# Kernel tuning notes

Hardware: AMD Instinct MI355X
Metric: run time of the kernel (lower is better)

Reference implementation:

```python
import jax, jax.numpy as jnp
import numpy as np

N_NODES = 100000
N_FEATURES = 128
N_FILTERS = 128
N_EDGES = 3200000


def setup_inputs() -> dict:
    key = jax.random.key(0)
    k_x, k_f, k_src, k_dst, k_w = jax.random.split(key, 5)
    x = jax.random.normal(k_x, (N_NODES, N_FEATURES), dtype=jnp.float32)
    filters = jax.random.normal(k_f, (N_FEATURES, N_FILTERS), dtype=jnp.float32)
    edge_src = jax.random.randint(k_src, (N_EDGES,), 0, N_NODES, dtype=jnp.int64)
    edge_dst = jnp.sort(jax.random.randint(k_dst, (N_EDGES,), 0, N_NODES, dtype=jnp.int64))
    edge_weight = jax.random.uniform(k_w, (N_EDGES,), dtype=jnp.float32)
    return {"x": x, "filters": filters, "edge_src": edge_src,
            "edge_dst": edge_dst, "edge_weight": edge_weight}


def reference(x, filters, edge_src, edge_dst, edge_weight):
    # Dense feature transform: XF = x @ filters  -> [N, n_filters]
    XF = jnp.matmul(x, filters)
    # Sparse aggregation: out[d] += w_e * XF[s] for each edge (s, d, w_e)
    # equivalent to torch.sparse.mm(transform, XF) with transform in COO form.
    msgs = XF[edge_src] * edge_weight[:, None]           # [E, n_filters]
    out = jax.ops.segment_sum(msgs, edge_dst, num_segments=N_NODES)
    return out
```

## Files before the change

kernel.cpp:

```cpp
#include <hip/hip_runtime.h>
#include <stdint.h>

#define N_NODES 100000
#define N_FEAT 128
#define N_EDGES 3200000

static __device__ __forceinline__ unsigned int f2bf_u(float f) {
    unsigned int u = __float_as_uint(f);
    u += 0x7FFFu + ((u >> 16) & 1u);
    return u >> 16;
}

typedef __bf16 bf16x8 __attribute__((ext_vector_type(8)));
typedef float f32x4 __attribute__((ext_vector_type(4)));

__global__ __launch_bounds__(256) void k_prep(
        const float* __restrict__ x, unsigned int* __restrict__ xi8,
        float* __restrict__ xscale,
        const float* __restrict__ f, unsigned short* __restrict__ fB,
        const int* __restrict__ dst, int* __restrict__ row_ptr) {
    int b = blockIdx.x;
    if (b < 12500) {
        int wave = threadIdx.x >> 6, lane = threadIdx.x & 63;
        int l32 = lane & 31;
        int node = b * 8 + wave * 2 + (lane >> 5);
        float4 v = *(const float4*)(x + (size_t)node * 128 + l32 * 4);
        float am = fmaxf(fmaxf(fabsf(v.x), fabsf(v.y)), fmaxf(fabsf(v.z), fabsf(v.w)));
        for (int d = 1; d < 32; d <<= 1) am = fmaxf(am, __shfl_xor(am, d));
        float s = am * (1.f / 127.f);
        float inv = 127.f / fmaxf(am, 1e-20f);
        int q0 = (int)rintf(v.x * inv), q1 = (int)rintf(v.y * inv);
        int q2 = (int)rintf(v.z * inv), q3 = (int)rintf(v.w * inv);
        xi8[(size_t)node * 32 + l32] = (unsigned int)((q0 & 0xFF) | ((q1 & 0xFF) << 8) |
                                                      ((q2 & 0xFF) << 16) | ((q3 & 0xFF) << 24));
        if (l32 == 0) xscale[node] = s;
    } else if (b < 25000) {
        int e = (b - 12500) * 256 + threadIdx.x;
        if (e >= N_EDGES) return;
        int dcur = dst[e];
        if (e == 0) {
            for (int d = 0; d <= dcur; ++d) row_ptr[d] = 0;
        } else {
            int dprev = dst[e - 1];
            for (int d = dprev + 1; d <= dcur; ++d) row_ptr[d] = e;
        }
        if (e == N_EDGES - 1) {
            for (int d = dcur + 1; d <= N_NODES; ++d) row_ptr[d] = N_EDGES;
        }
    } else {
        int i = (b - 25000) * 256 + threadIdx.x;
        if (i >= N_FEAT * N_FEAT) return;
        int n = ((i >> 11) << 4) | ((i >> 3) & 15);
        int k = (((i >> 9) & 3) << 5) | (((i >> 7) & 3) << 3) | (i & 7);
        fB[i] = (unsigned short)f2bf_u(f[k * 128 + n]);
    }
}

__global__ __launch_bounds__(256) void k_aggregate(
        const unsigned int* __restrict__ xi8,
        const float* __restrict__ xscale,
        const int* __restrict__ src,
        const float* __restrict__ w,
        const int* __restrict__ row_ptr,
        unsigned int* __restrict__ aggb) {
    __shared__ uint2 smeta[4][64];
    int wave = threadIdx.x >> 6, lane = threadIdx.x & 63;
    int node = blockIdx.x * 4 + wave;
    if (node >= N_NODES) return;
    int half = lane >> 5, f = lane & 31;
    int start = row_ptr[node], end = row_ptr[node + 1];
    float a0 = 0.f, a1 = 0.f, a2 = 0.f, a3 = 0.f;

    for (int e0 = start; e0 < end; e0 += 64) {
        int e = e0 + lane;
        uint2 m = make_uint2(0u, 0u);
        if (e < end) {
            int sv = src[e];
            m.x = (unsigned int)sv;
            m.y = __float_as_uint(w[e] * xscale[sv]);
        }
        smeta[wave][lane] = m;
        int cnt16 = (min(64, end - e0) + 15) & ~15;
        for (int j = 0; j < cnt16; j += 16) {
            unsigned int vv[8]; float wj[8];
#pragma unroll
            for (int u = 0; u < 8; ++u) {
                uint2 mm = smeta[wave][j + u * 2 + half];
                wj[u] = __uint_as_float(mm.y);
                vv[u] = xi8[mm.x * 32 + f];
            }
#pragma unroll
            for (int u = 0; u < 8; ++u) {
                int s32 = (int)vv[u];
                a0 = fmaf(wj[u], (float)((s32 << 24) >> 24), a0);
                a1 = fmaf(wj[u], (float)((s32 << 16) >> 24), a1);
                a2 = fmaf(wj[u], (float)((s32 <<  8) >> 24), a2);
                a3 = fmaf(wj[u], (float)( s32        >> 24), a3);
            }
        }
    }
    a0 += __shfl_xor(a0, 32);
    a1 += __shfl_xor(a1, 32);
    a2 += __shfl_xor(a2, 32);
    a3 += __shfl_xor(a3, 32);
    if (half == 0) {
        uint2 o;
        o.x = (f2bf_u(a1) << 16) | f2bf_u(a0);
        o.y = (f2bf_u(a3) << 16) | f2bf_u(a2);
        *(uint2*)(aggb + (size_t)node * 64 + f * 2) = o;
    }
}

__global__ __launch_bounds__(256) void k_gemm(
        const unsigned short* __restrict__ A,
        const unsigned short* __restrict__ fB,
        float* __restrict__ C) {
    __shared__ unsigned short Bbuf[16384];
    int t = threadIdx.x;
    for (int i = 0; i < 8; ++i)
        ((uint4*)Bbuf)[t + i * 256] = ((const uint4*)fB)[t + i * 256];
    __syncthreads();

    int wave = t >> 6, lane = t & 63, m15 = lane & 15, q = lane >> 4;
    int row = blockIdx.x * 64 + wave * 16 + m15;
    int rowc = min(row, N_NODES - 1);

    f32x4 acc[8];
#pragma unroll
    for (int j = 0; j < 8; ++j) acc[j] = f32x4{0.f, 0.f, 0.f, 0.f};

#pragma unroll
    for (int kkidx = 0; kkidx < 4; ++kkidx) {
        bf16x8 a = *(const bf16x8*)(A + (size_t)rowc * 128 + kkidx * 32 + q * 8);
#pragma unroll
        for (int j = 0; j < 8; ++j) {
            bf16x8 b = *(const bf16x8*)(Bbuf + (((j * 4 + kkidx) * 64 + lane) * 8));
            acc[j] = __builtin_amdgcn_mfma_f32_16x16x32_bf16(a, b, acc[j], 0, 0, 0);
        }
    }

    int rowbase = blockIdx.x * 64 + wave * 16 + q * 4;
#pragma unroll
    for (int j = 0; j < 8; ++j)
        for (int r = 0; r < 4; ++r) {
            int gr = rowbase + r;
            if (gr < N_NODES)
                C[(size_t)gr * 128 + j * 16 + m15] = acc[j][r];
        }
}

extern "C" void kernel_launch(void* const* d_in, const int* in_sizes, int n_in,
                              void* d_out, int out_size, void* d_ws, size_t ws_size,
                              hipStream_t stream) {
    const float* x        = (const float*)d_in[0];
    const float* filters  = (const float*)d_in[1];
    const int*   edge_src = (const int*)d_in[2];
    const int*   edge_dst = (const int*)d_in[3];
    const float* edge_w   = (const float*)d_in[4];
    float* out = (float*)d_out;

    char* ws = (char*)d_ws;
    unsigned int*   xi8  = (unsigned int*)  (ws);
    float*          xsc  = (float*)         (ws + 13ll * 1024 * 1024);
    unsigned int*   aggb = (unsigned int*)  (ws + 14ll * 1024 * 1024);
    unsigned short* fB   = (unsigned short*)(ws + 40ll * 1024 * 1024);
    int*            rp   = (int*)           (ws + 41ll * 1024 * 1024);

    hipLaunchKernelGGL(k_prep, dim3(25064), dim3(256), 0, stream,
                       x, xi8, xsc, filters, fB, edge_dst, rp);
    hipLaunchKernelGGL(k_aggregate, dim3(25000), dim3(256), 0, stream,
                       xi8, xsc, edge_src, edge_w, rp, aggb);
    hipLaunchKernelGGL(k_gemm, dim3(1563), dim3(256), 0, stream,
                       (const unsigned short*)aggb, fB, out);
}
```

Measured before the change: 201.9 us.

## Reorder to transform-then-aggregate with int8-quantized XF and direct fp32 output

Moves the dense matmul ahead of the sparse aggregation: a new kernel computes XF = x @ filters with bf16 MFMA and quantizes each row to offset-128 uint8 with a per-row scale. The aggregation kernel then gathers the int8 XF rows, subtracts the offset using an accumulated weight sum, and writes fp32 output directly. This removes the separate GEMM pass and the bf16 intermediate aggregate buffer, at the cost of quantizing XF rather than x, which changes the error profile.

```diff
diff --git a/kernel.cpp b/kernel.cpp
--- a/kernel.cpp
+++ b/kernel.cpp
@@ -15,27 +15,11 @@
 typedef float f32x4 __attribute__((ext_vector_type(4)));
 
 __global__ __launch_bounds__(256) void k_prep(
-        const float* __restrict__ x, unsigned int* __restrict__ xi8,
-        float* __restrict__ xscale,
         const float* __restrict__ f, unsigned short* __restrict__ fB,
         const int* __restrict__ dst, int* __restrict__ row_ptr) {
     int b = blockIdx.x;
     if (b < 12500) {
-        int wave = threadIdx.x >> 6, lane = threadIdx.x & 63;
-        int l32 = lane & 31;
-        int node = b * 8 + wave * 2 + (lane >> 5);
-        float4 v = *(const float4*)(x + (size_t)node * 128 + l32 * 4);
-        float am = fmaxf(fmaxf(fabsf(v.x), fabsf(v.y)), fmaxf(fabsf(v.z), fabsf(v.w)));
-        for (int d = 1; d < 32; d <<= 1) am = fmaxf(am, __shfl_xor(am, d));
-        float s = am * (1.f / 127.f);
-        float inv = 127.f / fmaxf(am, 1e-20f);
-        int q0 = (int)rintf(v.x * inv), q1 = (int)rintf(v.y * inv);
-        int q2 = (int)rintf(v.z * inv), q3 = (int)rintf(v.w * inv);
-        xi8[(size_t)node * 32 + l32] = (unsigned int)((q0 & 0xFF) | ((q1 & 0xFF) << 8) |
-                                                      ((q2 & 0xFF) << 16) | ((q3 & 0xFF) << 24));
-        if (l32 == 0) xscale[node] = s;
-    } else if (b < 25000) {
-        int e = (b - 12500) * 256 + threadIdx.x;
+        int e = b * 256 + threadIdx.x;
         if (e >= N_EDGES) return;
         int dcur = dst[e];
         if (e == 0) {
@@ -48,11 +32,76 @@
             for (int d = dcur + 1; d <= N_NODES; ++d) row_ptr[d] = N_EDGES;
         }
     } else {
-        int i = (b - 25000) * 256 + threadIdx.x;
+        int i = (b - 12500) * 256 + threadIdx.x;
         if (i >= N_FEAT * N_FEAT) return;
         int n = ((i >> 11) << 4) | ((i >> 3) & 15);
         int k = (((i >> 9) & 3) << 5) | (((i >> 7) & 3) << 3) | (i & 7);
         fB[i] = (unsigned short)f2bf_u(f[k * 128 + n]);
+    }
+}
+
+__global__ __launch_bounds__(256) void k_xf(
+        const float* __restrict__ x,
+        const unsigned short* __restrict__ fB,
+        unsigned int* __restrict__ xi8,
+        float* __restrict__ xscale) {
+    __shared__ unsigned short Bbuf[16384];
+    int t = threadIdx.x;
+    for (int i = 0; i < 8; ++i)
+        ((uint4*)Bbuf)[t + i * 256] = ((const uint4*)fB)[t + i * 256];
+    __syncthreads();
+
+    int wave = t >> 6, lane = t & 63, m15 = lane & 15, q = lane >> 4;
+    int row = blockIdx.x * 64 + wave * 16 + m15;
+    int rowc = min(row, N_NODES - 1);
+
+    f32x4 acc[8];
+#pragma unroll
+    for (int j = 0; j < 8; ++j) acc[j] = f32x4{0.f, 0.f, 0.f, 0.f};
+
+#pragma unroll
+    for (int kkidx = 0; kkidx < 4; ++kkidx) {
+        const float* ap = x + (size_t)rowc * 128 + kkidx * 32 + q * 8;
+        float4 v0 = *(const float4*)ap;
+        float4 v1 = *(const float4*)(ap + 4);
+        union { bf16x8 v; unsigned short s[8]; } au;
+        au.s[0] = (unsigned short)f2bf_u(v0.x);
+        au.s[1] = (unsigned short)f2bf_u(v0.y);
+        au.s[2] = (unsigned short)f2bf_u(v0.z);
+        au.s[3] = (unsigned short)f2bf_u(v0.w);
+        au.s[4] = (unsigned short)f2bf_u(v1.x);
+        au.s[5] = (unsigned short)f2bf_u(v1.y);
+        au.s[6] = (unsigned short)f2bf_u(v1.z);
+        au.s[7] = (unsigned short)f2bf_u(v1.w);
+#pragma unroll
+        for (int j = 0; j < 8; ++j) {
+            bf16x8 bfrag = *(const bf16x8*)(Bbuf + (((j * 4 + kkidx) * 64 + lane) * 8));
+            acc[j] = __builtin_amdgcn_mfma_f32_16x16x32_bf16(au.v, bfrag, acc[j], 0, 0, 0);
+        }
+    }
+
+    int rowbase = blockIdx.x * 64 + wave * 16 + q * 4;
+#pragma unroll
+    for (int r = 0; r < 4; ++r) {
+        float mx = 0.f;
+#pragma unroll
+        for (int j = 0; j < 8; ++j) mx = fmaxf(mx, fabsf(acc[j][r]));
+        for (int d = 1; d < 16; d <<= 1) mx = fmaxf(mx, __shfl_xor(mx, d));
+        float inv = 127.f / fmaxf(mx, 1e-20f);
+        unsigned int u0 = 0, u1 = 0;
+#pragma unroll
+        for (int bb = 0; bb < 4; ++bb) {
+            unsigned int q0 = (unsigned int)(int)(rintf(acc[2 * bb][r] * inv) + 128.f);
+            unsigned int q1 = (unsigned int)(int)(rintf(acc[2 * bb + 1][r] * inv) + 128.f);
+            u0 |= (q0 & 0xFFu) << (8 * bb);
+            u1 |= (q1 & 0xFFu) << (8 * bb);
+        }
+        int gr = rowbase + r;
+        if (gr < N_NODES) {
+            xi8[(size_t)gr * 32 + m15] = u0;
+            xi8[(size_t)gr * 32 + 16 + m15] = u1;
+            if (m15 == 0) xscale[gr] = mx * (1.f / 127.f);
+        }
     }
 }
 
@@ -62,14 +111,14 @@
         const int* __restrict__ src,
         const float* __restrict__ w,
         const int* __restrict__ row_ptr,
-        unsigned int* __restrict__ aggb) {
+        float* __restrict__ out) {
     __shared__ uint2 smeta[4][64];
     int wave = threadIdx.x >> 6, lane = threadIdx.x & 63;
     int node = blockIdx.x * 4 + wave;
     if (node >= N_NODES) return;
     int half = lane >> 5, f = lane & 31;
     int start = row_ptr[node], end = row_ptr[node + 1];
-    float a0 = 0.f, a1 = 0.f, a2 = 0.f, a3 = 0.f;
+    float a0 = 0.f, a1 = 0.f, a2 = 0.f, a3 = 0.f, aw = 0.f;
 
     for (int e0 = start; e0 < end; e0 += 64) {
         int e = e0 + lane;
@@ -91,62 +140,30 @@
             }
 #pragma unroll
             for (int u = 0; u < 8; ++u) {
-                int s32 = (int)vv[u];
-                a0 = fmaf(wj[u], (float)((s32 << 24) >> 24), a0);
-                a1 = fmaf(wj[u], (float)((s32 << 16) >> 24), a1);
-                a2 = fmaf(wj[u], (float)((s32 <<  8) >> 24), a2);
-                a3 = fmaf(wj[u], (float)( s32        >> 24), a3);
+                a0 = fmaf(wj[u], (float)( vv[u]         & 0xFFu), a0);
+                a1 = fmaf(wj[u], (float)((vv[u] >>  8)  & 0xFFu), a1);
+                a2 = fmaf(wj[u], (float)((vv[u] >> 16)  & 0xFFu), a2);
+                a3 = fmaf(wj[u], (float)( vv[u] >> 24          ), a3);
+                aw += wj[u];
             }
         }
     }
+    a0 = fmaf(-128.f, aw, a0);
+    a1 = fmaf(-128.f, aw, a1);
+    a2 = fmaf(-128.f, aw, a2);
+    a3 = fmaf(-128.f, aw, a3);
+
     a0 += __shfl_xor(a0, 32);
     a1 += __shfl_xor(a1, 32);
     a2 += __shfl_xor(a2, 32);
     a3 += __shfl_xor(a3, 32);
     if (half == 0) {
-        uint2 o;
-        o.x = (f2bf_u(a1) << 16) | f2bf_u(a0);
-        o.y = (f2bf_u(a3) << 16) | f2bf_u(a2);
-        *(uint2*)(aggb + (size_t)node * 64 + f * 2) = o;
+        float* o = out + (size_t)node * 128 + f;
+        o[ 0] = a0;
+        o[32] = a1;
+        o[64] = a2;
+        o[96] = a3;
     }
-}
-
-__global__ __launch_bounds__(256) void k_gemm(
-        const unsigned short* __restrict__ A,
-        const unsigned short* __restrict__ fB,
-        float* __restrict__ C) {
-    __shared__ unsigned short Bbuf[16384];
-    int t = threadIdx.x;
-    for (int i = 0; i < 8; ++i)
-        ((uint4*)Bbuf)[t + i * 256] = ((const uint4*)fB)[t + i * 256];
-    __syncthreads();
-
-    int wave = t >> 6, lane = t & 63, m15 = lane & 15, q = lane >> 4;
-    int row = blockIdx.x * 64 + wave * 16 + m15;
-    int rowc = min(row, N_NODES - 1);
-
-    f32x4 acc[8];
-#pragma unroll
-    for (int j = 0; j < 8; ++j) acc[j] = f32x4{0.f, 0.f, 0.f, 0.f};
-
-#pragma unroll
-    for (int kkidx = 0; kkidx < 4; ++kkidx) {
-        bf16x8 a = *(const bf16x8*)(A + (size_t)rowc * 128 + kkidx * 32 + q * 8);
-#pragma unroll
-        for (int j = 0; j < 8; ++j) {
-            bf16x8 b = *(const bf16x8*)(Bbuf + (((j * 4 + kkidx) * 64 + lane) * 8));
-            acc[j] = __builtin_amdgcn_mfma_f32_16x16x32_bf16(a, b, acc[j], 0, 0, 0);
-        }
-    }
-
-    int rowbase = blockIdx.x * 64 + wave * 16 + q * 4;
-#pragma unroll
-    for (int j = 0; j < 8; ++j)
-        for (int r = 0; r < 4; ++r) {
-            int gr = rowbase + r;
-            if (gr < N_NODES)
-                C[(size_t)gr * 128 + j * 16 + m15] = acc[j][r];
-        }
 }
 
 extern "C" void kernel_launch(void* const* d_in, const int* in_sizes, int n_in,
@@ -160,16 +177,15 @@
     float* out = (float*)d_out;
 
     char* ws = (char*)d_ws;
-    unsigned int*   xi8  = (unsigned int*)  (ws);
-    float*          xsc  = (float*)         (ws + 13ll * 1024 * 1024);
-    unsigned int*   aggb = (unsigned int*)  (ws + 14ll * 1024 * 1024);
-    unsigned short* fB   = (unsigned short*)(ws + 40ll * 1024 * 1024);
-    int*            rp   = (int*)           (ws + 41ll * 1024 * 1024);
+    unsigned int*   xi8 = (unsigned int*)  (ws);
+    float*          xsc = (float*)         (ws + 13ll * 1024 * 1024);
+    unsigned short* fB  = (unsigned short*)(ws + 14ll * 1024 * 1024);
+    int*            rp  = (int*)           (ws + 15ll * 1024 * 1024);
 
-    hipLaunchKernelGGL(k_prep, dim3(25064), dim3(256), 0, stream,
-                       x, xi8, xsc, filters, fB, edge_dst, rp);
+    hipLaunchKernelGGL(k_prep, dim3(12564), dim3(256), 0, stream,
+                       filters, fB, edge_dst, rp);
+    hipLaunchKernelGGL(k_xf, dim3(1563), dim3(256), 0, stream,
+                       x, fB, xi8, xsc);
     hipLaunchKernelGGL(k_aggregate, dim3(25000), dim3(256), 0, stream,
-                       xi8, xsc, edge_src, edge_w, rp, aggb);
-    hipLaunchKernelGGL(k_gemm, dim3(1563), dim3(256), 0, stream,
-                       (const unsigned short*)aggb, fB, out);
+                       xi8, xsc, edge_src, edge_w, rp, out);
 }
```

Measured after the change: 196.1 us. 1.03x faster.
